# Performance work log

Measured on AMD Instinct MI355X. Metric: run time of the kernel, lower is better.

Reference implementation:

```python
import jax, jax.numpy as jnp
import numpy as np

B, C_I, C_O, K, H, W = 8, 64, 64, 3, 256, 256
GROUPS = 16  # int(c_o / min(4, c_o)) = 64/4
EPS = 1e-5
PAD = K  # pad_x = pad_y = k + (bc-1) with bc_x=bc_y=1, k=3


def _conv(x, w):
    # x: (B, C_i, h, w), w: (C_o, C_i, K, K), valid conv, stride 1
    return jax.lax.conv_general_dilated(
        x, w, window_strides=(1, 1), padding='VALID',
        dimension_numbers=('NCHW', 'OIHW', 'NCHW'))


def setup_inputs() -> dict:
    key = jax.random.key(0)
    ks = jax.random.split(key, 10)
    s = 1.0 / np.sqrt(C_I * K * K)  # torch Conv2d default init bound
    wshape = (C_O, C_I, K, K)
    names = ['w_int', 'w_tl', 'w_tr', 'w_bl', 'w_br', 'w_top', 'w_bot', 'w_left', 'w_right']
    d = {'x': jax.random.normal(ks[0], (B, C_I, H, W), dtype=jnp.float32)}
    for i, n in enumerate(names):
        d[n] = jax.random.uniform(ks[i + 1], wshape, jnp.float32, -s, s)
    d['bias'] = jnp.zeros((1, C_O, 1, 1), jnp.float32)   # learnable_bias (init zeros)
    d['gamma'] = jnp.ones((C_O,), jnp.float32)           # GroupNorm weight
    d['beta'] = jnp.zeros((C_O,), jnp.float32)           # GroupNorm bias
    return d


def reference(x, w_int, w_tl, w_tr, w_bl, w_br, w_top, w_bot, w_left, w_right, bias, gamma, beta):
    p = PAD
    # corners -> (B,C,1,1)
    tl = _conv(x[:, :, :p, :p], w_tl)
    tr = _conv(x[:, :, :p, -p:], w_tr)
    bl = _conv(x[:, :, -p:, :p], w_bl)
    br = _conv(x[:, :, -p:, -p:], w_br)
    # edges -> (B,C,1,W-2) / (B,C,H-2,1)
    top = _conv(x[:, :, :p, :], w_top)
    bot = _conv(x[:, :, -p:, :], w_bot)
    left = _conv(x[:, :, :, :p], w_left)
    right = _conv(x[:, :, :, -p:], w_right)
    # interior -> (B,C,H-2,W-2)
    mid = _conv(x, w_int)
    mid = jnp.concatenate([left, mid, right], axis=3)       # (B,C,H-2,W)
    top_row = jnp.concatenate([tl, top, tr], axis=3)        # (B,C,1,W)
    bot_row = jnp.concatenate([bl, bot, br], axis=3)        # (B,C,1,W)
    # NOTE: original code puts the 'bottom' conv output first along dim 2
    y = jnp.concatenate([bot_row, mid, top_row], axis=2) + bias  # (B,C,H,W)
    # GroupNorm(16, 64)
    yg = y.reshape(B, GROUPS, -1)
    mu = jnp.mean(yg, axis=2, keepdims=True)
    var = jnp.var(yg, axis=2, keepdims=True)
    yn = ((yg - mu) * jax.lax.rsqrt(var + EPS)).reshape(B, C_O, H, W)
    yn = yn * gamma[None, :, None, None] + beta[None, :, None, None]
    # SELU activation; dropout(rate=0) is identity
    return jax.nn.selu(yn)
```

## Files before the change

### kernel.cpp

```cpp
#include <hip/hip_runtime.h>

#define B_ 8
#define CI 64
#define CO 64
#define H_ 256
#define W_ 256
#define EPS_ 1e-5f

#define SELU_SCALE 1.0507009873554805f
#define SELU_SA    1.7580993408473766f

typedef __attribute__((ext_vector_type(8))) short short8;
typedef __attribute__((ext_vector_type(4))) float f32x4;

__device__ __forceinline__ unsigned short f2bf(float f) {
    unsigned int u = __float_as_uint(f);
    u = (u + 0x7fffu + ((u >> 16) & 1u)) >> 16;
    return (unsigned short)u;
}
__device__ __forceinline__ float bf2f(unsigned short h) {
    return __uint_as_float(((unsigned)h) << 16);
}

__global__ __launch_bounds__(256) void prepass_weights(
    const float* __restrict__ w_int,
    const float* __restrict__ w_bl, const float* __restrict__ w_br,
    const float* __restrict__ w_tl, const float* __restrict__ w_tr,
    const float* __restrict__ w_bot, const float* __restrict__ w_top,
    const float* __restrict__ w_left, const float* __restrict__ w_right,
    unsigned short* __restrict__ wpre, float* __restrict__ wedge)
{
    const int blk = blockIdx.x, t = threadIdx.x;
    if (blk < 72) {
        const int wid = blk / 9, pos = blk % 9;
        const float* src = (wid == 0) ? w_bl : (wid == 1) ? w_br
                         : (wid == 2) ? w_tl : (wid == 3) ? w_tr
                         : (wid == 4) ? w_bot : (wid == 5) ? w_top
                         : (wid == 6) ? w_left : w_right;
        float* dst = wedge + (size_t)blk * 4096;
        for (int k = 0; k < 16; ++k) {
            const int lin = k * 256 + t;
            const int c4  = lin >> 8;
            const int co  = (lin >> 2) & 63;
            const int j   = lin & 3;
            const int ci  = c4 * 4 + j;
            dst[lin] = src[(co * 64 + ci) * 9 + pos];
        }
    } else {
        const int pos = blk - 72;
        for (int k = 0; k < 16; ++k) {
            const int lin = k * 256 + t;
            const int co = lin >> 6, cip = lin & 63;
            const int ci = cip ^ ((co & 7) << 3);
            wpre[pos * 4096 + lin] = f2bf(w_int[(co * 64 + ci) * 9 + pos]);
        }
    }
}

__global__ __launch_bounds__(256) void prepass_x(
    const float* __restrict__ x, unsigned short* __restrict__ xpre)
{
    __shared__ unsigned short ls[256 * 72];
    const int row = blockIdx.x, b = blockIdx.y;
    const int t = threadIdx.x;
    const int colq = t >> 2;
    const float* xb = x + ((size_t)(b * 64) * 256 + row) * 256;

    for (int sp = 0; sp < 4; ++sp) {
        const int cibase = sp * 16 + (t & 3) * 4;
        float4 v[4];
#pragma unroll
        for (int e = 0; e < 4; ++e)
            v[e] = *(const float4*)(xb + (size_t)(cibase + e) * 65536 + colq * 4);
#pragma unroll
        for (int jj = 0; jj < 4; ++jj) {
            const int col = colq * 4 + jj;
            const int sw  = (col & 7) << 3;
            ushort4 pk;
            pk.x = f2bf((&v[0].x)[jj]);
            pk.y = f2bf((&v[1].x)[jj]);
            pk.z = f2bf((&v[2].x)[jj]);
            pk.w = f2bf((&v[3].x)[jj]);
            *(ushort4*)&ls[col * 72 + (cibase ^ sw)] = pk;
        }
    }
    __syncthreads();
    unsigned short* xp = xpre + ((size_t)(b * 256 + row)) * 256 * 64;
    for (int q = 0; q < 8; ++q) {
        const int lin = q * 256 + t;
        const int col = lin >> 3, k = lin & 7;
        *(uint4*)(xp + col * 64 + k * 8) = *(const uint4*)&ls[col * 72 + k * 8];
    }
}

__global__ __launch_bounds__(512) void conv_mfma(
    const unsigned short* __restrict__ xpre, const unsigned short* __restrict__ wpre,
    const float* __restrict__ bias, float* __restrict__ y,
    float* __restrict__ part)
{
    __shared__ unsigned short xs[10 * 48 * 64];
    __shared__ unsigned short wl[9 * 64 * 64];
    __shared__ float sred[8][16][2];
    const int t = threadIdx.x, w = t >> 6, lane = t & 63;
    const int b = blockIdx.z, r0 = blockIdx.y * 8, c0 = blockIdx.x * 32;

    for (int L = w; L < 60; L += 8) {
        const int j = L / 6, i = L % 6;
        int rr = r0 - 1 + j; rr = rr < 0 ? 0 : (rr > 255 ? 255 : rr);
        int col = c0 - 8 + i * 8 + (lane >> 3);
        col = col < 0 ? 0 : (col > 255 ? 255 : col);
        uint4 v = *(const uint4*)((const char*)xpre +
                    ((size_t)((b * 256 + rr) * 256 + col)) * 128 + (lane & 7) * 16);
        *(uint4*)((char*)xs + j * 6144 + i * 1024 + lane * 16) = v;
    }
    for (int L = w * 9; L < w * 9 + 9; ++L) {
        uint4 v = *(const uint4*)((const char*)wpre + L * 1024 + lane * 16);
        *(uint4*)((char*)wl + L * 1024 + lane * 16) = v;
    }
    __syncthreads();

    f32x4 acc[4][2];
#pragma unroll
    for (int m = 0; m < 4; ++m)
#pragma unroll
        for (int n = 0; n < 2; ++n)
            acc[m][n] = (f32x4){0.f, 0.f, 0.f, 0.f};

    const int l15 = lane & 15, lg = lane >> 4;
#pragma unroll
    for (int pos = 0; pos < 9; ++pos) {
        const int kr = pos / 3, kc = pos % 3;
        const int j = w + kr;
#pragma unroll
        for (int ks = 0; ks < 2; ++ks) {
            const int cib = ks * 32 + lg * 8;
            short8 bf[2], af[4];
#pragma unroll
            for (int n = 0; n < 2; ++n) {
                const int s = n * 16 + l15 + kc + 7;
                bf[n] = *(const short8*)&xs[j * 3072 + s * 64 + (cib ^ ((s & 7) << 3))];
            }
#pragma unroll
            for (int m = 0; m < 4; ++m) {
                const int co = m * 16 + l15;
                af[m] = *(const short8*)&wl[pos * 4096 + co * 64 + (cib ^ ((co & 7) << 3))];
            }
#pragma unroll
            for (int m = 0; m < 4; ++m)
#pragma unroll
                for (int n = 0; n < 2; ++n)
                    acc[m][n] = __builtin_amdgcn_mfma_f32_16x16x32_bf16(
                        af[m], bf[n], acc[m][n], 0, 0, 0);
        }
    }

    const int r = r0 + w;
    const bool rmask = (r != 0) && (r != 255);
    float s4[4] = {0.f, 0.f, 0.f, 0.f}, q4[4] = {0.f, 0.f, 0.f, 0.f};
#pragma unroll
    for (int m = 0; m < 4; ++m)
#pragma unroll
        for (int n = 0; n < 2; ++n) {
            const int c = c0 + n * 16 + l15;
            const bool pmask = rmask && (c != 0) && (c != 255);
#pragma unroll
            for (int reg = 0; reg < 4; ++reg) {
                const int co = m * 16 + lg * 4 + reg;
                const float v = acc[m][n][reg] + bias[co];
                y[(((size_t)b * 64 + co) * 256 + r) * 256 + c] = v;
                if (pmask) { s4[m] += v; q4[m] += v * v; }
            }
        }
#pragma unroll
    for (int off = 1; off < 16; off <<= 1)
#pragma unroll
        for (int m = 0; m < 4; ++m) {
            s4[m] += __shfl_xor(s4[m], off);
            q4[m] += __shfl_xor(q4[m], off);
        }
    if (l15 == 0) {
#pragma unroll
        for (int m = 0; m < 4; ++m) {
            sred[w][m * 4 + lg][0] = s4[m];
            sred[w][m * 4 + lg][1] = q4[m];
        }
    }
    __syncthreads();
    if (t < 32) {
        const int g = t & 15, sel = t >> 4;
        float v = 0.f;
#pragma unroll
        for (int ww = 0; ww < 8; ++ww) v += sred[ww][g][sel];
        const int slot = blockIdx.y * 8 + blockIdx.x;
        part[((size_t)(b * 512 + slot) * 16 + g) * 2 + sel] = v;
    }
}

__global__ __launch_bounds__(256) void conv_edge2(
    const unsigned short* __restrict__ xpre, const float* __restrict__ wedge,
    const float* __restrict__ bias, float* __restrict__ y,
    float* __restrict__ part)
{
    __shared__ float xl[4][9][64];
    __shared__ float ered[4][16][2];
    const int b = blockIdx.x, edge = blockIdx.y, seg = blockIdx.z;
    const int t = threadIdx.x, p = t >> 6, lane = t & 63;

    for (int unit = t; unit < 288; unit += 256) {
        const int chunk = unit >> 3, sub = unit & 7;
        const int pp = chunk / 9, rem = chunk % 9, kr = rem / 3, kc = rem % 3;
        int e = seg * 4 + pp;
        if (edge >= 2 && e > 253) e = 253;
        int row, colb;
        if (edge == 0)      { row = 253 + kr; colb = (e == 0) ? 0 : ((e == 255) ? 253 : (e - 1)); }
        else if (edge == 1) { row = kr;       colb = (e == 0) ? 0 : ((e == 255) ? 253 : (e - 1)); }
        else if (edge == 2) { row = e + kr;   colb = 0; }
        else                { row = e + kr;   colb = 253; }
        const int col = colb + kc;
        const uint4 v = *(const uint4*)(xpre +
            ((size_t)((b * 256 + row) * 256 + col)) * 64 + sub * 8);
        const int ci0 = (sub ^ (col & 7)) * 8;
        float* dst = &xl[pp][kr * 3 + kc][ci0];
        const unsigned short* hv = (const unsigned short*)&v;
#pragma unroll
        for (int j = 0; j < 8; ++j) dst[j] = bf2f(hv[j]);
    }
    __syncthreads();

    int e = seg * 4 + p;
    const bool active = (edge < 2) || (e <= 253);
    if (edge >= 2 && e > 253) e = 253;
    int wid, r_out, c_out;
    if (edge == 0)      { wid = (e == 0) ? 0 : ((e == 255) ? 1 : 4); r_out = 0;   c_out = e; }
    else if (edge == 1) { wid = (e == 0) ? 2 : ((e == 255) ? 3 : 5); r_out = 255; c_out = e; }
    else if (edge == 2) { wid = 6; r_out = e + 1; c_out = 0; }
    else                { wid = 7; r_out = e + 1; c_out = 255; }

    const int co = lane;
    float acc = 0.f;
    const float* wbase = wedge + (size_t)wid * 36864;
#pragma unroll
    for (int pos = 0; pos < 9; ++pos) {
        const float* wp = wbase + pos * 4096 + lane * 4;
        const float* xp = &xl[p][pos][0];
#pragma unroll
        for (int c4 = 0; c4 < 16; ++c4) {
            const float4 wv = *(const float4*)(wp + c4 * 256);
            const float4 xv = *(const float4*)(xp + c4 * 4);
            acc = fmaf(wv.x, xv.x, acc); acc = fmaf(wv.y, xv.y, acc);
            acc = fmaf(wv.z, xv.z, acc); acc = fmaf(wv.w, xv.w, acc);
        }
    }
    const float v = acc + bias[co];
    if (active) y[(((size_t)b * 64 + co) * 256 + r_out) * 256 + c_out] = v;
    float s = active ? v : 0.f, q = active ? v * v : 0.f;
    s += __shfl_xor(s, 1); q += __shfl_xor(q, 1);
    s += __shfl_xor(s, 2); q += __shfl_xor(q, 2);
    if ((lane & 3) == 0) { ered[p][co >> 2][0] = s; ered[p][co >> 2][1] = q; }
    __syncthreads();
    if (t < 32) {
        const int g = t & 15, sel = t >> 4;
        const float r = ered[0][g][sel] + ered[1][g][sel] +
                        ered[2][g][sel] + ered[3][g][sel];
        const int slot = 256 + (edge * 64 + seg);
        part[((size_t)(b * 512 + slot) * 16 + g) * 2 + sel] = r;
    }
}

__global__ __launch_bounds__(256) void stats_reduce(
    const float* __restrict__ part, float* __restrict__ mv)
{
    __shared__ float sred[16][16][2];
    const int b = blockIdx.x, t = threadIdx.x;
    const int g = t & 15, chunk = t >> 4;
    float s = 0.f, q = 0.f;
    for (int k = 0; k < 32; ++k) {
        const int slot = chunk * 32 + k;
        const size_t base = ((size_t)(b * 512 + slot) * 16 + g) * 2;
        s += part[base]; q += part[base + 1];
    }
    sred[chunk][g][0] = s; sred[chunk][g][1] = q;
    __syncthreads();
    if (t < 16) {
        float S = 0.f, Q = 0.f;
#pragma unroll
        for (int c = 0; c < 16; ++c) { S += sred[c][t][0]; Q += sred[c][t][1]; }
        const float inv_n = 1.0f / (4.0f * 65536.0f);
        const float mean = S * inv_n;
        const float var  = Q * inv_n - mean * mean;
        mv[(b * 16 + t) * 2]     = mean;
        mv[(b * 16 + t) * 2 + 1] = rsqrtf(var + EPS_);
    }
}

__global__ __launch_bounds__(256) void norm_mv(
    float* __restrict__ y, const float* __restrict__ mv,
    const float* __restrict__ gamma, const float* __restrict__ beta)
{
    const size_t tt = (size_t)blockIdx.x * 256 + threadIdx.x;
    const size_t e = tt * 4;
    const int b  = (int)(e >> 22);
    const int ch = (int)((e >> 16) & 63);
    const int g  = ch >> 2;
    const float mean = mv[(b * 16 + g) * 2];
    const float rstd = mv[(b * 16 + g) * 2 + 1];
    const float ga = gamma[ch] * rstd;
    const float be = beta[ch] - mean * ga;
    float4 v = reinterpret_cast<float4*>(y)[tt];
    float u;
    u = v.x * ga + be; v.x = (u > 0.f) ? SELU_SCALE * u : SELU_SA * (__expf(u) - 1.f);
    u = v.y * ga + be; v.y = (u > 0.f) ? SELU_SCALE * u : SELU_SA * (__expf(u) - 1.f);
    u = v.z * ga + be; v.z = (u > 0.f) ? SELU_SCALE * u : SELU_SA * (__expf(u) - 1.f);
    u = v.w * ga + be; v.w = (u > 0.f) ? SELU_SCALE * u : SELU_SA * (__expf(u) - 1.f);
    reinterpret_cast<float4*>(y)[tt] = v;
}

__global__ __launch_bounds__(256) void conv_main(
    const float* __restrict__ x, const float* __restrict__ w,
    const float* __restrict__ bias, float* __restrict__ y)
{
    const int c = threadIdx.x;
    const int r = blockIdx.x;
    const int b = blockIdx.y;
    const int rr = (r == 0) ? (H_ - 3) : ((r == H_ - 1) ? 0 : (r - 1));
    const int cc = min(max(c - 1, 0), W_ - 3);
    float acc[CO];
#pragma unroll
    for (int co = 0; co < CO; ++co) acc[co] = 0.f;
    const float* xb = x + (size_t)b * CI * H_ * W_;
    for (int ci = 0; ci < CI; ++ci) {
        const float* xp = xb + ((size_t)ci * H_ + rr) * W_ + cc;
        float xv[9];
#pragma unroll
        for (int kr = 0; kr < 3; ++kr)
#pragma unroll
            for (int kc = 0; kc < 3; ++kc)
                xv[kr * 3 + kc] = xp[kr * W_ + kc];
        const float* wci = w + ci * 9;
#pragma unroll
        for (int co = 0; co < CO; ++co) {
            const float* wp = wci + co * (CI * 9);
            float a = acc[co];
#pragma unroll
            for (int k = 0; k < 9; ++k) a = fmaf(xv[k], wp[k], a);
            acc[co] = a;
        }
    }
#pragma unroll
    for (int co = 0; co < CO; ++co)
        y[(((size_t)b * CO + co) * H_ + r) * W_ + c] = acc[co] + bias[co];
}

__global__ __launch_bounds__(256) void conv_edge(
    const float* __restrict__ x,
    const float* __restrict__ w_bot, const float* __restrict__ w_top,
    const float* __restrict__ w_left, const float* __restrict__ w_right,
    const float* __restrict__ bias, float* __restrict__ y)
{
    const int b     = blockIdx.x;
    const int edge  = blockIdx.y;
    const int seg   = blockIdx.z;
    const int el    = threadIdx.x & 63;
    const int chunk = threadIdx.x >> 6;
    const int e     = seg * 64 + el;
    const bool active = (e < 254);
    const int ec    = active ? e : 253;
    const float* w = (edge == 0) ? w_bot : (edge == 1) ? w_top
                   : (edge == 2) ? w_left : w_right;
    int r_out, c_out, rr, cc;
    if (edge == 0)      { r_out = 0;      c_out = 1 + ec; rr = H_ - 3; cc = ec; }
    else if (edge == 1) { r_out = H_ - 1; c_out = 1 + ec; rr = 0;      cc = ec; }
    else if (edge == 2) { r_out = 1 + ec; c_out = 0;      rr = ec;     cc = 0; }
    else                { r_out = 1 + ec; c_out = W_ - 1; rr = ec;     cc = W_ - 3; }
    float acc[CO];
#pragma unroll
    for (int co = 0; co < CO; ++co) acc[co] = 0.f;
    const float* xb = x + (size_t)b * CI * H_ * W_;
    const int ci0 = chunk * 16;
    for (int ci = ci0; ci < ci0 + 16; ++ci) {
        const float* xp = xb + ((size_t)ci * H_ + rr) * W_ + cc;
        float xv[9];
#pragma unroll
        for (int kr = 0; kr < 3; ++kr)
#pragma unroll
            for (int kc = 0; kc < 3; ++kc)
                xv[kr * 3 + kc] = xp[kr * W_ + kc];
#pragma unroll
        for (int co = 0; co < CO; ++co) {
            const float* wp = w + co * (CI * 9) + ci * 9;
            float a = acc[co];
#pragma unroll
            for (int k = 0; k < 9; ++k) a = fmaf(xv[k], wp[k], a);
            acc[co] = a;
        }
    }
    __shared__ float lds[64][65];
    for (int s = 0; s < 4; ++s) {
        if (chunk == s) {
            if (s == 0) {
#pragma unroll
                for (int co = 0; co < CO; ++co) lds[el][co] = acc[co];
            } else {
#pragma unroll
                for (int co = 0; co < CO; ++co) lds[el][co] += acc[co];
            }
        }
        __syncthreads();
    }
    if (chunk == 0 && active) {
#pragma unroll
        for (int co = 0; co < CO; ++co)
            y[(((size_t)b * CO + co) * H_ + r_out) * W_ + c_out] = lds[el][co] + bias[co];
    }
}

__global__ __launch_bounds__(256) void conv_corner(
    const float* __restrict__ x,
    const float* __restrict__ w_bl, const float* __restrict__ w_br,
    const float* __restrict__ w_tl, const float* __restrict__ w_tr,
    const float* __restrict__ bias, float* __restrict__ y)
{
    const int b      = blockIdx.x;
    const int corner = threadIdx.x >> 6;
    const int co     = threadIdx.x & 63;
    const float* w = (corner == 0) ? w_bl : (corner == 1) ? w_br
                   : (corner == 2) ? w_tl : w_tr;
    const int rr    = (corner < 2) ? (H_ - 3) : 0;
    const int cc    = (corner & 1) ? (W_ - 3) : 0;
    const int r_out = (corner < 2) ? 0 : (H_ - 1);
    const int c_out = (corner & 1) ? (W_ - 1) : 0;
    const float* xb = x + (size_t)b * CI * H_ * W_;
    float a = 0.f;
    for (int ci = 0; ci < CI; ++ci) {
        const float* xp = xb + ((size_t)ci * H_ + rr) * W_ + cc;
        const float* wp = w + ((size_t)co * CI + ci) * 9;
#pragma unroll
        for (int kr = 0; kr < 3; ++kr)
#pragma unroll
            for (int kc = 0; kc < 3; ++kc)
                a = fmaf(xp[kr * W_ + kc], wp[kr * 3 + kc], a);
    }
    y[(((size_t)b * CO + co) * H_ + r_out) * W_ + c_out] = a + bias[co];
}

__global__ __launch_bounds__(256) void stats_kernel(
    const float* __restrict__ y, float* __restrict__ ws)
{
    const int bid   = blockIdx.x;
    const int chunk = bid & 3;
    const int g     = (bid >> 2) & 15;
    const int b     = bid >> 6;
    const float* p  = y + ((size_t)(b * 64 + g * 4 + chunk)) * (H_ * W_);
    float s = 0.f, q = 0.f;
    for (int i = threadIdx.x; i < (H_ * W_ / 4); i += 256) {
        float4 v = reinterpret_cast<const float4*>(p)[i];
        s += v.x + v.y + v.z + v.w;
        q += v.x * v.x + v.y * v.y + v.z * v.z + v.w * v.w;
    }
#pragma unroll
    for (int off = 32; off; off >>= 1) {
        s += __shfl_down(s, off);
        q += __shfl_down(q, off);
    }
    __shared__ float red[8];
    const int wid = threadIdx.x >> 6;
    if ((threadIdx.x & 63) == 0) { red[wid * 2] = s; red[wid * 2 + 1] = q; }
    __syncthreads();
    if (threadIdx.x == 0) {
        ws[bid * 2]     = red[0] + red[2] + red[4] + red[6];
        ws[bid * 2 + 1] = red[1] + red[3] + red[5] + red[7];
    }
}

__global__ __launch_bounds__(256) void norm_stats(
    float* __restrict__ y, const float* __restrict__ st,
    const float* __restrict__ gamma, const float* __restrict__ beta)
{
    const size_t t = (size_t)blockIdx.x * 256 + threadIdx.x;
    const size_t e = t * 4;
    const int b  = (int)(e >> 22);
    const int ch = (int)((e >> 16) & 63);
    const int g  = ch >> 2;
    const int sb = ((b * 16 + g) * 4) * 2;
    const float S = st[sb] + st[sb + 2] + st[sb + 4] + st[sb + 6];
    const float Q = st[sb + 1] + st[sb + 3] + st[sb + 5] + st[sb + 7];
    const float inv_n = 1.0f / (4.0f * H_ * W_);
    const float mean  = S * inv_n;
    const float var   = Q * inv_n - mean * mean;
    const float rstd  = rsqrtf(var + EPS_);
    const float ga = gamma[ch] * rstd;
    const float be = beta[ch] - mean * ga;
    float4 v = reinterpret_cast<float4*>(y)[t];
    float u;
    u = v.x * ga + be; v.x = (u > 0.f) ? SELU_SCALE * u : SELU_SA * (__expf(u) - 1.f);
    u = v.y * ga + be; v.y = (u > 0.f) ? SELU_SCALE * u : SELU_SA * (__expf(u) - 1.f);
    u = v.z * ga + be; v.z = (u > 0.f) ? SELU_SCALE * u : SELU_SA * (__expf(u) - 1.f);
    u = v.w * ga + be; v.w = (u > 0.f) ? SELU_SCALE * u : SELU_SA * (__expf(u) - 1.f);
    reinterpret_cast<float4*>(y)[t] = v;
}

extern "C" void kernel_launch(void* const* d_in, const int* in_sizes, int n_in,
                              void* d_out, int out_size, void* d_ws, size_t ws_size,
                              hipStream_t stream) {
    const float* x       = (const float*)d_in[0];
    const float* w_int   = (const float*)d_in[1];
    const float* w_tl    = (const float*)d_in[2];
    const float* w_tr    = (const float*)d_in[3];
    const float* w_bl    = (const float*)d_in[4];
    const float* w_br    = (const float*)d_in[5];
    const float* w_top   = (const float*)d_in[6];
    const float* w_bot   = (const float*)d_in[7];
    const float* w_left  = (const float*)d_in[8];
    const float* w_right = (const float*)d_in[9];
    const float* bias    = (const float*)d_in[10];
    const float* gamma   = (const float*)d_in[11];
    const float* beta    = (const float*)d_in[12];

    float* y = (float*)d_out;

    const size_t XPRE  = 67108864ull;
    const size_t WPRE  = 73728ull;
    const size_t WEDGE = 1179648ull;
    const size_t PART  = 524288ull;
    const size_t MV    = 1024ull;
    const size_t NEED  = XPRE + WPRE + WEDGE + PART + MV;

    if (ws_size >= NEED) {
        unsigned short* xpre = (unsigned short*)d_ws;
        unsigned short* wpre = (unsigned short*)((char*)d_ws + XPRE);
        float* wedge = (float*)((char*)d_ws + XPRE + WPRE);
        float* part  = (float*)((char*)d_ws + XPRE + WPRE + WEDGE);
        float* mv    = (float*)((char*)d_ws + XPRE + WPRE + WEDGE + PART);

        prepass_weights<<<dim3(81), 256, 0, stream>>>(
            w_int, w_bl, w_br, w_tl, w_tr, w_bot, w_top, w_left, w_right, wpre, wedge);
        prepass_x<<<dim3(256, 8), 256, 0, stream>>>(x, xpre);
        conv_mfma<<<dim3(8, 32, 8), 512, 0, stream>>>(xpre, wpre, bias, y, part);
        conv_edge2<<<dim3(8, 4, 64), 256, 0, stream>>>(xpre, wedge, bias, y, part);
        stats_reduce<<<dim3(8), 256, 0, stream>>>(part, mv);
        norm_mv<<<dim3(32768), 256, 0, stream>>>(y, mv, gamma, beta);
    } else {
        float* stats = (float*)d_ws;
        conv_main<<<dim3(H_, B_), 256, 0, stream>>>(x, w_int, bias, y);
        conv_edge<<<dim3(B_, 4, 4), 256, 0, stream>>>(x, w_bot, w_top, w_left, w_right, bias, y);
        conv_corner<<<dim3(B_), 256, 0, stream>>>(x, w_bl, w_br, w_tl, w_tr, bias, y);
        stats_kernel<<<dim3(512), 256, 0, stream>>>(y, stats);
        norm_stats<<<dim3(32768), 256, 0, stream>>>(y, stats, gamma, beta);
    }
}
```

Measured before the change: 202.1 us.

## Store pre-norm conv output as bf16 and read weights directly from global

The conv kernels now write the pre-normalization activations to a bf16 workspace buffer instead of fp32 into the output. The norm/SELU pass reads 8 bf16 values per thread and writes fp32 to the output, which halves the intermediate write and read traffic. The conv_mfma weight tile is no longer staged in LDS; fragments are loaded from global/L1 directly, and launch bounds now request 4 blocks per CU so the freed LDS allows more occupancy. This needs an extra 64MB of workspace and rounds intermediates to bf16, which costs accuracy.

```diff
diff --git a/kernel.cpp b/kernel.cpp
--- a/kernel.cpp
+++ b/kernel.cpp
@@ -20,6 +20,9 @@
 }
 __device__ __forceinline__ float bf2f(unsigned short h) {
     return __uint_as_float(((unsigned)h) << 16);
+}
+__device__ __forceinline__ float selu_f(float u) {
+    return (u > 0.f) ? SELU_SCALE * u : SELU_SA * (__expf(u) - 1.f);
 }
 
 __global__ __launch_bounds__(256) void prepass_weights(
@@ -93,13 +96,12 @@
     }
 }
 
-__global__ __launch_bounds__(512) void conv_mfma(
+__global__ __launch_bounds__(512, 4) void conv_mfma(
     const unsigned short* __restrict__ xpre, const unsigned short* __restrict__ wpre,
-    const float* __restrict__ bias, float* __restrict__ y,
+    const float* __restrict__ bias, unsigned short* __restrict__ ybf,
     float* __restrict__ part)
 {
     __shared__ unsigned short xs[10 * 48 * 64];
-    __shared__ unsigned short wl[9 * 64 * 64];
     __shared__ float sred[8][16][2];
     const int t = threadIdx.x, w = t >> 6, lane = t & 63;
     const int b = blockIdx.z, r0 = blockIdx.y * 8, c0 = blockIdx.x * 32;
@@ -113,10 +115,6 @@
                     ((size_t)((b * 256 + rr) * 256 + col)) * 128 + (lane & 7) * 16);
         *(uint4*)((char*)xs + j * 6144 + i * 1024 + lane * 16) = v;
     }
-    for (int L = w * 9; L < w * 9 + 9; ++L) {
-        uint4 v = *(const uint4*)((const char*)wpre + L * 1024 + lane * 16);
-        *(uint4*)((char*)wl + L * 1024 + lane * 16) = v;
-    }
     __syncthreads();
 
     f32x4 acc[4][2];
@@ -127,6 +125,7 @@
             acc[m][n] = (f32x4){0.f, 0.f, 0.f, 0.f};
 
     const int l15 = lane & 15, lg = lane >> 4;
+    const int sw15 = (l15 & 7) << 3;
 #pragma unroll
     for (int pos = 0; pos < 9; ++pos) {
         const int kr = pos / 3, kc = pos % 3;
@@ -134,6 +133,7 @@
 #pragma unroll
         for (int ks = 0; ks < 2; ++ks) {
             const int cib = ks * 32 + lg * 8;
+            const unsigned short* wp = wpre + pos * 4096 + l15 * 64 + (cib ^ sw15);
             short8 bf[2], af[4];
 #pragma unroll
             for (int n = 0; n < 2; ++n) {
@@ -141,10 +141,8 @@
                 bf[n] = *(const short8*)&xs[j * 3072 + s * 64 + (cib ^ ((s & 7) << 3))];
             }
 #pragma unroll
-            for (int m = 0; m < 4; ++m) {
-                const int co = m * 16 + l15;
-                af[m] = *(const short8*)&wl[pos * 4096 + co * 64 + (cib ^ ((co & 7) << 3))];
-            }
+            for (int m = 0; m < 4; ++m)
+                af[m] = *(const short8*)(wp + m * 1024);
 #pragma unroll
             for (int m = 0; m < 4; ++m)
 #pragma unroll
@@ -167,7 +165,7 @@
             for (int reg = 0; reg < 4; ++reg) {
                 const int co = m * 16 + lg * 4 + reg;
                 const float v = acc[m][n][reg] + bias[co];
-                y[(((size_t)b * 64 + co) * 256 + r) * 256 + c] = v;
+                ybf[(((size_t)b * 64 + co) * 256 + r) * 256 + c] = f2bf(v);
                 if (pmask) { s4[m] += v; q4[m] += v * v; }
             }
         }
@@ -198,7 +196,7 @@
 
 __global__ __launch_bounds__(256) void conv_edge2(
     const unsigned short* __restrict__ xpre, const float* __restrict__ wedge,
-    const float* __restrict__ bias, float* __restrict__ y,
+    const float* __restrict__ bias, unsigned short* __restrict__ ybf,
     float* __restrict__ part)
 {
     __shared__ float xl[4][9][64];
@@ -252,7 +250,7 @@
         }
     }
     const float v = acc + bias[co];
-    if (active) y[(((size_t)b * 64 + co) * 256 + r_out) * 256 + c_out] = v;
+    if (active) ybf[(((size_t)b * 64 + co) * 256 + r_out) * 256 + c_out] = f2bf(v);
     float s = active ? v : 0.f, q = active ? v * v : 0.f;
     s += __shfl_xor(s, 1); q += __shfl_xor(q, 1);
     s += __shfl_xor(s, 2); q += __shfl_xor(q, 2);
@@ -293,12 +291,13 @@
     }
 }
 
-__global__ __launch_bounds__(256) void norm_mv(
-    float* __restrict__ y, const float* __restrict__ mv,
+__global__ __launch_bounds__(256) void norm_bf(
+    const unsigned short* __restrict__ ybf, float* __restrict__ out,
+    const float* __restrict__ mv,
     const float* __restrict__ gamma, const float* __restrict__ beta)
 {
     const size_t tt = (size_t)blockIdx.x * 256 + threadIdx.x;
-    const size_t e = tt * 4;
+    const size_t e = tt * 8;
     const int b  = (int)(e >> 22);
     const int ch = (int)((e >> 16) & 63);
     const int g  = ch >> 2;
@@ -306,13 +305,20 @@
     const float rstd = mv[(b * 16 + g) * 2 + 1];
     const float ga = gamma[ch] * rstd;
     const float be = beta[ch] - mean * ga;
-    float4 v = reinterpret_cast<float4*>(y)[tt];
-    float u;
-    u = v.x * ga + be; v.x = (u > 0.f) ? SELU_SCALE * u : SELU_SA * (__expf(u) - 1.f);
-    u = v.y * ga + be; v.y = (u > 0.f) ? SELU_SCALE * u : SELU_SA * (__expf(u) - 1.f);
-    u = v.z * ga + be; v.z = (u > 0.f) ? SELU_SCALE * u : SELU_SA * (__expf(u) - 1.f);
-    u = v.w * ga + be; v.w = (u > 0.f) ? SELU_SCALE * u : SELU_SA * (__expf(u) - 1.f);
-    reinterpret_cast<float4*>(y)[tt] = v;
+
+    const uint4 v = *(const uint4*)(ybf + e);
+    float f[8];
+    f[0] = __uint_as_float(v.x << 16); f[1] = __uint_as_float(v.x & 0xffff0000u);
+    f[2] = __uint_as_float(v.y << 16); f[3] = __uint_as_float(v.y & 0xffff0000u);
+    f[4] = __uint_as_float(v.z << 16); f[5] = __uint_as_float(v.z & 0xffff0000u);
+    f[6] = __uint_as_float(v.w << 16); f[7] = __uint_as_float(v.w & 0xffff0000u);
+    float4 o0, o1;
+    o0.x = selu_f(f[0] * ga + be); o0.y = selu_f(f[1] * ga + be);
+    o0.z = selu_f(f[2] * ga + be); o0.w = selu_f(f[3] * ga + be);
+    o1.x = selu_f(f[4] * ga + be); o1.y = selu_f(f[5] * ga + be);
+    o1.z = selu_f(f[6] * ga + be); o1.w = selu_f(f[7] * ga + be);
+    *(float4*)(out + e)     = o0;
+    *(float4*)(out + e + 4) = o1;
 }
 
 __global__ __launch_bounds__(256) void conv_main(
@@ -492,10 +498,10 @@
     const float be = beta[ch] - mean * ga;
     float4 v = reinterpret_cast<float4*>(y)[t];
     float u;
-    u = v.x * ga + be; v.x = (u > 0.f) ? SELU_SCALE * u : SELU_SA * (__expf(u) - 1.f);
-    u = v.y * ga + be; v.y = (u > 0.f) ? SELU_SCALE * u : SELU_SA * (__expf(u) - 1.f);
-    u = v.z * ga + be; v.z = (u > 0.f) ? SELU_SCALE * u : SELU_SA * (__expf(u) - 1.f);
-    u = v.w * ga + be; v.w = (u > 0.f) ? SELU_SCALE * u : SELU_SA * (__expf(u) - 1.f);
+    u = v.x * ga + be; v.x = selu_f(u);
+    u = v.y * ga + be; v.y = selu_f(u);
+    u = v.z * ga + be; v.z = selu_f(u);
+    u = v.w * ga + be; v.w = selu_f(u);
     reinterpret_cast<float4*>(y)[t] = v;
 }
 
@@ -516,35 +522,37 @@
     const float* gamma   = (const float*)d_in[11];
     const float* beta    = (const float*)d_in[12];
 
-    float* y = (float*)d_out;
+    float* out = (float*)d_out;
 
     const size_t XPRE  = 67108864ull;
+    const size_t YBF   = 67108864ull;
     const size_t WPRE  = 73728ull;
     const size_t WEDGE = 1179648ull;
     const size_t PART  = 524288ull;
     const size_t MV    = 1024ull;
-    const size_t NEED  = XPRE + WPRE + WEDGE + PART + MV;
+    const size_t NEED  = XPRE + YBF + WPRE + WEDGE + PART + MV;
 
     if (ws_size >= NEED) {
         unsigned short* xpre = (unsigned short*)d_ws;
-        unsigned short* wpre = (unsigned short*)((char*)d_ws + XPRE);
-        float* wedge = (float*)((char*)d_ws + XPRE + WPRE);
-        float* part  = (float*)((char*)d_ws + XPRE + WPRE + WEDGE);
-        float* mv    = (float*)((char*)d_ws + XPRE + WPRE + WEDGE + PART);
+        unsigned short* ybf  = (unsigned short*)((char*)d_ws + XPRE);
+        unsigned short* wpre = (unsigned short*)((char*)d_ws + XPRE + YBF);
+        float* wedge = (float*)((char*)d_ws + XPRE + YBF + WPRE);
+        float* part  = (float*)((char*)d_ws + XPRE + YBF + WPRE + WEDGE);
+        float* mv    = (float*)((char*)d_ws + XPRE + YBF + WPRE + WEDGE + PART);
 
         prepass_weights<<<dim3(81), 256, 0, stream>>>(
             w_int, w_bl, w_br, w_tl, w_tr, w_bot, w_top, w_left, w_right, wpre, wedge);
         prepass_x<<<dim3(256, 8), 256, 0, stream>>>(x, xpre);
-        conv_mfma<<<dim3(8, 32, 8), 512, 0, stream>>>(xpre, wpre, bias, y, part);
-        conv_edge2<<<dim3(8, 4, 64), 256, 0, stream>>>(xpre, wedge, bias, y, part);
+        conv_mfma<<<dim3(8, 32, 8), 512, 0, stream>>>(xpre, wpre, bias, ybf, part);
+        conv_edge2<<<dim3(8, 4, 64), 256, 0, stream>>>(xpre, wedge, bias, ybf, part);
         stats_reduce<<<dim3(8), 256, 0, stream>>>(part, mv);
-        norm_mv<<<dim3(32768), 256, 0, stream>>>(y, mv, gamma, beta);
+        norm_bf<<<dim3(16384), 256, 0, stream>>>(ybf, out, mv, gamma, beta);
     } else {
         float* stats = (float*)d_ws;
-        conv_main<<<dim3(H_, B_), 256, 0, stream>>>(x, w_int, bias, y);
-        conv_edge<<<dim3(B_, 4, 4), 256, 0, stream>>>(x, w_bot, w_top, w_left, w_right, bias, y);
-        conv_corner<<<dim3(B_), 256, 0, stream>>>(x, w_bl, w_br, w_tl, w_tr, bias, y);
-        stats_kernel<<<dim3(512), 256, 0, stream>>>(y, stats);
-        norm_stats<<<dim3(32768), 256, 0, stream>>>(y, stats, gamma, beta);
-    }
-}
+        conv_main<<<dim3(H_, B_), 256, 0, stream>>>(x, w_int, bias, out);
+        conv_edge<<<dim3(B_, 4, 4), 256, 0, stream>>>(x, w_bot, w_top, w_left, w_right, bias, out);
+        conv_corner<<<dim3(B_), 256, 0, stream>>>(x, w_bl, w_br, w_tl, w_tr, bias, out);
+        stats_kernel<<<dim3(512), 256, 0, stream>>>(out, stats);
+        norm_stats<<<dim3(32768), 256, 0, stream>>>(out, stats, gamma, beta);
+    }
+}
```

Result: no change. 200.9 us (-0.6%).
